# Optimization experiments

Measured on AMD Instinct MI355X. Metric: run time of the kernel, lower is better.

The kernel has to match this reference:

```python
import jax, jax.numpy as jnp
import numpy as np
import math

N_DRUG, N_DIS, D, EMB, HEADS, STEPS = 3072, 3072, 64, 16, 4, 5
N = N_DRUG + N_DIS


def setup_inputs() -> dict:
    key = jax.random.key(0)
    ks = jax.random.split(key, 16)
    s = lambda fan: 1.0 / np.sqrt(fan)
    return {
        "graph": jax.random.uniform(ks[0], (N, N), jnp.float32),
        "drug_f": jax.random.normal(ks[1], (N_DRUG, D), jnp.float32),
        "disease_f": jax.random.normal(ks[2], (N_DIS, D), jnp.float32),
        "timesteps": jax.random.randint(ks[3], (N,), 0, STEPS, jnp.int32),
        "drug_w": jax.random.normal(ks[4], (D, D), jnp.float32) * s(D),
        "disease_w": jax.random.normal(ks[5], (D, D), jnp.float32) * s(D),
        "emb_w": jax.random.normal(ks[6], (EMB, EMB), jnp.float32) * s(EMB),
        "emb_b": jnp.zeros((EMB,), jnp.float32),
        "in_w": jax.random.normal(ks[7], (D + EMB, 256), jnp.float32) * s(D + EMB),
        "in_b": jnp.zeros((256,), jnp.float32),
        "out_w": jax.random.normal(ks[8], (256, D), jnp.float32) * s(256),
        "out_b": jnp.zeros((D,), jnp.float32),
        "wq": jax.random.normal(ks[9], (D, D), jnp.float32) * s(D),
        "bq": jnp.zeros((D,), jnp.float32),
        "wk": jax.random.normal(ks[10], (D, D), jnp.float32) * s(D),
        "bk": jnp.zeros((D,), jnp.float32),
        "wv": jax.random.normal(ks[11], (D, D), jnp.float32) * s(D),
        "bv": jnp.zeros((D,), jnp.float32),
        "wo": jax.random.normal(ks[12], (D, D), jnp.float32) * s(D),
        "bo": jnp.zeros((D,), jnp.float32),
        "fuse_w": jax.random.normal(ks[13], (2 * D, D), jnp.float32) * s(2 * D),
        "fuse_b": jnp.zeros((D,), jnp.float32),
        "ln_g": jnp.ones((D,), jnp.float32),
        "ln_b": jnp.zeros((D,), jnp.float32),
    }


def _layernorm(x, g, b, eps=1e-5):
    mu = jnp.mean(x, axis=-1, keepdims=True)
    var = jnp.var(x, axis=-1, keepdims=True)
    return (x - mu) * jax.lax.rsqrt(var + eps) * g + b


def reference(graph, drug_f, disease_f, timesteps, drug_w, disease_w,
              emb_w, emb_b, in_w, in_b, out_w, out_b,
              wq, bq, wk, bk, wv, bv, wo, bo,
              fuse_w, fuse_b, ln_g, ln_b):
    # ---- DGLLayer: per-type projection + symmetric degree-norm propagation ----
    node_f = jnp.concatenate([drug_f @ drug_w, disease_f @ disease_w], axis=0)  # [N, D]
    degs = jnp.clip(jnp.sum(graph, axis=1), 1.0, None)
    norm = jax.lax.rsqrt(degs)[:, None]  # degs^-0.5, [N, 1]
    target = (graph @ (node_f * norm)) * norm

    # ---- Denoise MLP with sinusoidal time embedding ----
    half = EMB // 2
    freqs = jnp.exp(-math.log(10000.0) * jnp.arange(half, dtype=jnp.float32) / half)
    temp = timesteps.astype(jnp.float32)[:, None] * freqs[None]  # [N, half]
    time_emb = jnp.concatenate([jnp.cos(temp), jnp.sin(temp)], axis=-1)  # [N, EMB]
    emb = time_emb @ emb_w + emb_b
    h = jnp.concatenate([target, emb], axis=-1)  # [N, D+EMB]
    h = jnp.tanh(h @ in_w + in_b)  # in-layer
    aux = h @ out_w + out_b        # final out-layer (no tanh)

    # ---- AttentionFusion: cross-attention(target -> aux) + fuse + residual LN ----
    hd = D // HEADS
    q = (target @ wq + bq).reshape(N, HEADS, hd)
    k = (aux @ wk + bk).reshape(N, HEADS, hd)
    v = (aux @ wv + bv).reshape(N, HEADS, hd)
    scores = jnp.einsum('nhd,mhd->hnm', q, k) / np.sqrt(hd)  # [H, N, N]
    attn = jax.nn.softmax(scores, axis=-1)
    attn_out = jnp.einsum('hnm,mhd->nhd', attn, v).reshape(N, D) @ wo + bo
    fused = jnp.concatenate([target, attn_out], axis=-1) @ fuse_w + fuse_b
    return _layernorm(fused + target, ln_g, ln_b)
```

## Files before the change

### kernel.cpp

```cpp
#include <hip/hip_runtime.h>
#include <cstdint>
#include <cstddef>

#define NTOT 6144
#define NDRUG 3072
#define NM (NTOT*64)

typedef __fp16 f16;
typedef __attribute__((ext_vector_type(2))) __fp16 f16x2;
typedef __attribute__((ext_vector_type(4))) __fp16 f16x4;
typedef __attribute__((ext_vector_type(8))) __fp16 f16x8;
typedef __attribute__((ext_vector_type(4))) float f32x4;

__device__ __forceinline__ f16x8 pack8(float4 a, float4 b){
  f16x2 p0 = __builtin_amdgcn_cvt_pkrtz(a.x, a.y);
  f16x2 p1 = __builtin_amdgcn_cvt_pkrtz(a.z, a.w);
  f16x2 p2 = __builtin_amdgcn_cvt_pkrtz(b.x, b.y);
  f16x2 p3 = __builtin_amdgcn_cvt_pkrtz(b.z, b.w);
  f16x4 lo = __builtin_shufflevector(p0, p1, 0, 1, 2, 3);
  f16x4 hi = __builtin_shufflevector(p2, p3, 0, 1, 2, 3);
  return __builtin_shufflevector(lo, hi, 0, 1, 2, 3, 4, 5, 6, 7);
}

__global__ __launch_bounds__(256) void k_deg(const float* __restrict__ g,
                                             const float* __restrict__ drug_f,
                                             const float* __restrict__ dis_f,
                                             const float* __restrict__ drug_w,
                                             const float* __restrict__ dis_w,
                                             float* __restrict__ norm,
                                             f16* __restrict__ nfst){
  __shared__ float sx[4][64];
  __shared__ float snf[4][64];
  int wv = threadIdx.x >> 6, j = threadIdx.x & 63;
  int row = blockIdx.x*4 + wv;
  const float4* p = (const float4*)(g + (size_t)row * NTOT);
  float s = 0.f;
  #pragma unroll
  for (int it = 0; it < 24; ++it) {
    float4 u = p[it*64 + j];
    s += (u.x + u.y) + (u.z + u.w);
  }
  #pragma unroll
  for (int off = 32; off; off >>= 1) s += __shfl_xor(s, off, 64);
  float nrm = rsqrtf(fmaxf(s, 1.0f));
  if (j == 0) norm[row] = nrm;

  const float* x; const float* W;
  if (row < NDRUG){ x = drug_f + (size_t)row*64; W = drug_w; }
  else            { x = dis_f + (size_t)(row-NDRUG)*64; W = dis_w; }
  sx[wv][j] = x[j];
  __syncthreads();
  float acc = 0.f;
  #pragma unroll 8
  for (int k = 0; k < 64; ++k) acc = fmaf(sx[wv][k], W[k*64+j], acc);
  snf[wv][j] = acc * nrm;
  __syncthreads();
  if (threadIdx.x < 64){
    int c = threadIdx.x;
    f16x4 pk = {(f16)snf[0][c], (f16)snf[1][c], (f16)snf[2][c], (f16)snf[3][c]};
    *(f16x4*)(nfst + (size_t)c*NTOT + blockIdx.x*4) = pk;
  }
}

__global__ __launch_bounds__(256) void k_gemm(const float* __restrict__ graph,
                                              const f16* __restrict__ nfst,
                                              float* __restrict__ part){
  __shared__ f16 sA[2][64][72];
  __shared__ f16 sB[2][64][72];
  const int tid = threadIdx.x;
  const int lane = tid & 63, w = tid >> 6;
  const int l15 = lane & 15, quad = lane >> 4;
  const int row0 = blockIdx.x * 64;
  const int kbase = blockIdx.y * 768;
  const int sr = tid >> 2, scg = (tid & 3) * 16;

  f32x4 acc[4] = {{0.f,0.f,0.f,0.f},{0.f,0.f,0.f,0.f},
                  {0.f,0.f,0.f,0.f},{0.f,0.f,0.f,0.f}};
  float4 a0, a1, a2, a3;
  f16x8 rb0, rb1;
  auto LOADT = [&](int kt){
    const float4* pa = (const float4*)(graph + (size_t)(row0 + sr)*NTOT + kbase + kt*64 + scg);
    a0 = pa[0]; a1 = pa[1]; a2 = pa[2]; a3 = pa[3];
    const f16* pb = nfst + (size_t)sr*NTOT + kbase + kt*64 + scg;
    rb0 = *(const f16x8*)pb; rb1 = *(const f16x8*)(pb + 8);
  };
  auto WRITET = [&](int b){
    *(f16x8*)&sA[b][sr][scg]     = pack8(a0, a1);
    *(f16x8*)&sA[b][sr][scg + 8] = pack8(a2, a3);
    *(f16x8*)&sB[b][sr][scg]     = rb0;
    *(f16x8*)&sB[b][sr][scg + 8] = rb1;
  };
  LOADT(0); WRITET(0);
  int cur = 0;
  for (int kt = 0; kt < 12; ++kt){
    if (kt < 11) LOADT(kt + 1);
    __syncthreads();
    #pragma unroll
    for (int k16 = 0; k16 < 4; ++k16){
      f16x4 af = *(const f16x4*)&sA[cur][w*16 + l15][k16*16 + quad*4];
      #pragma unroll
      for (int nt = 0; nt < 4; ++nt){
        f16x4 bf = *(const f16x4*)&sB[cur][nt*16 + l15][k16*16 + quad*4];
        acc[nt] = __builtin_amdgcn_mfma_f32_16x16x16f16(af, bf, acc[nt], 0, 0, 0);
      }
    }
    if (kt < 11) WRITET(cur ^ 1);
    cur ^= 1;
  }
  float* dst = part + (size_t)blockIdx.y * NM;
  #pragma unroll
  for (int nt = 0; nt < 4; ++nt){
    #pragma unroll
    for (int r = 0; r < 4; ++r){
      int row = row0 + w*16 + quad*4 + r;
      dst[(size_t)row*64 + nt*16 + l15] = acc[nt][r];
    }
  }
}

__global__ __launch_bounds__(256) void k_node2(const float* __restrict__ part,
                                               const float* __restrict__ norm,
                                               const int* __restrict__ ts,
                                               const float* __restrict__ emb_w,
                                               const float* __restrict__ emb_b,
                                               const float* __restrict__ in_w,
                                               const float* __restrict__ in_b,
                                               const float* __restrict__ out_w,
                                               const float* __restrict__ out_b,
                                               const float* __restrict__ wq, const float* __restrict__ bq,
                                               const float* __restrict__ wk, const float* __restrict__ bk,
                                               const float* __restrict__ wvw, const float* __restrict__ bv,
                                               float* __restrict__ target,
                                               f16* __restrict__ qh, f16* __restrict__ kh,
                                               f16* __restrict__ vt){
  __shared__ float sx[4][80];
  __shared__ float sh[4][256];
  __shared__ float sa[4][64];
  __shared__ float sv[4][64];
  int wv = threadIdx.x>>6, j = threadIdx.x&63;
  int row = blockIdx.x*4 + wv;

  float t = 0.f;
  #pragma unroll
  for (int p = 0; p < 8; ++p) t += part[(size_t)p*NM + (size_t)row*64 + j];
  t *= norm[row];
  target[(size_t)row*64 + j] = t;
  sx[wv][j] = t;
  if (j < 16) {
    const float FREQ[8] = {1.0f, 0.316227766016838f, 0.1f, 0.0316227766016838f,
                           0.01f, 0.00316227766016838f, 0.001f, 0.000316227766016838f};
    float tt = (float)ts[row];
    float e = emb_b[j];
    #pragma unroll
    for (int k = 0; k < 8; ++k) {
      float a = tt * FREQ[k];
      e = fmaf(cosf(a), emb_w[k*16 + j], e);
      e = fmaf(sinf(a), emb_w[(8+k)*16 + j], e);
    }
    sx[wv][64 + j] = e;
  }
  __syncthreads();
  float a0 = in_b[4*j+0], a1 = in_b[4*j+1], a2 = in_b[4*j+2], a3 = in_b[4*j+3];
  #pragma unroll 8
  for (int k = 0; k < 80; ++k) {
    float xv = sx[wv][k];
    float4 w = *(const float4*)(in_w + k*256 + 4*j);
    a0 = fmaf(xv, w.x, a0);
    a1 = fmaf(xv, w.y, a1);
    a2 = fmaf(xv, w.z, a2);
    a3 = fmaf(xv, w.w, a3);
  }
  sh[wv][4*j+0] = tanhf(a0); sh[wv][4*j+1] = tanhf(a1);
  sh[wv][4*j+2] = tanhf(a2); sh[wv][4*j+3] = tanhf(a3);
  __syncthreads();
  float o = out_b[j];
  #pragma unroll 8
  for (int k = 0; k < 256; ++k) o = fmaf(sh[wv][k], out_w[k*64 + j], o);
  sa[wv][j] = o;
  __syncthreads();
  float q = bq[j], kk = bk[j], vv = bv[j];
  #pragma unroll 8
  for (int k = 0; k < 64; ++k) {
    float tv = sx[wv][k], av = sa[wv][k];
    q  = fmaf(tv, wq[k*64+j],  q);
    kk = fmaf(av, wk[k*64+j],  kk);
    vv = fmaf(av, wvw[k*64+j], vv);
  }
  qh[(size_t)row*64+j] = (f16)(q * 0.360673760222241f);
  kh[(size_t)row*64+j] = (f16)kk;
  sv[wv][j] = vv;
  __syncthreads();
  if (threadIdx.x < 64){
    int c = threadIdx.x;
    f16x4 pk = {(f16)sv[0][c], (f16)sv[1][c], (f16)sv[2][c], (f16)sv[3][c]};
    *(f16x4*)(vt + (size_t)c*NTOT + blockIdx.x*4) = pk;
  }
}

__global__ __launch_bounds__(256) void k_attn(const f16* __restrict__ qh,
                                              const f16* __restrict__ kh,
                                              const f16* __restrict__ vt,
                                              float* __restrict__ opart,
                                              float* __restrict__ lpart){
  __shared__ f16 sK[2][64][72];
  __shared__ f16 sV[2][64][72];
  const int tid = threadIdx.x;
  const int h = tid >> 6;
  const int lane = tid & 63;
  const int l15 = lane & 15, quad = lane >> 4;
  const int z = blockIdx.y;
  const int q0 = blockIdx.x * 64;

  f16x4 qf[4];
  #pragma unroll
  for (int qn = 0; qn < 4; ++qn)
    qf[qn] = *(const f16x4*)(qh + (size_t)(q0 + qn*16 + l15)*64 + h*16 + quad*4);

  f32x4 accOT[4] = {{0.f,0.f,0.f,0.f},{0.f,0.f,0.f,0.f},
                    {0.f,0.f,0.f,0.f},{0.f,0.f,0.f,0.f}};
  float lsum[4] = {0.f, 0.f, 0.f, 0.f};
  const int sr = tid >> 2, scg = (tid & 3) * 16;
  const int kbase = z * 768;
  f16x8 rk0, rk1, rv0, rv1;
  auto LOADT = [&](int kt){
    const int k0 = kbase + kt*64;
    const f16* pk = kh + (size_t)(k0 + sr)*64 + scg;
    rk0 = *(const f16x8*)pk; rk1 = *(const f16x8*)(pk + 8);
    const f16* pv = vt + (size_t)sr*NTOT + k0 + scg;
    rv0 = *(const f16x8*)pv; rv1 = *(const f16x8*)(pv + 8);
  };
  auto WRITET = [&](int b){
    *(f16x8*)&sK[b][sr][scg]     = rk0;
    *(f16x8*)&sK[b][sr][scg + 8] = rk1;
    *(f16x8*)&sV[b][sr][scg]     = rv0;
    *(f16x8*)&sV[b][sr][scg + 8] = rv1;
  };
  LOADT(0); WRITET(0);
  int cur = 0;
  for (int kt = 0; kt < 12; ++kt){
    if (kt < 11) LOADT(kt + 1);
    __syncthreads();
    #pragma unroll
    for (int km = 0; km < 4; ++km){
      f16x4 kf = *(const f16x4*)&sK[cur][km*16 + l15][h*16 + quad*4];
      f16x4 vf = *(const f16x4*)&sV[cur][h*16 + l15][km*16 + quad*4];
      #pragma unroll
      for (int qn = 0; qn < 4; ++qn){
        f32x4 s = __builtin_amdgcn_mfma_f32_16x16x16f16(
            kf, qf[qn], (f32x4){0.f,0.f,0.f,0.f}, 0, 0, 0);
        float p0 = exp2f(fminf(s[0], 14.4269504088896f));
        float p1 = exp2f(fminf(s[1], 14.4269504088896f));
        float p2 = exp2f(fminf(s[2], 14.4269504088896f));
        float p3 = exp2f(fminf(s[3], 14.4269504088896f));
        lsum[qn] += (p0 + p1) + (p2 + p3);
        f16x2 plo = __builtin_amdgcn_cvt_pkrtz(p0, p1);
        f16x2 phi = __builtin_amdgcn_cvt_pkrtz(p2, p3);
        f16x4 pf = __builtin_shufflevector(plo, phi, 0, 1, 2, 3);
        accOT[qn] = __builtin_amdgcn_mfma_f32_16x16x16f16(vf, pf, accOT[qn], 0, 0, 0);
      }
    }
    if (kt < 11) WRITET(cur ^ 1);
    cur ^= 1;
  }
  #pragma unroll
  for (int qn = 0; qn < 4; ++qn){
    lsum[qn] += __shfl_xor(lsum[qn], 16, 64);
    lsum[qn] += __shfl_xor(lsum[qn], 32, 64);
  }
  #pragma unroll
  for (int qn = 0; qn < 4; ++qn){
    const int row = q0 + qn*16 + l15;
    *(float4*)(opart + (size_t)z*NM + (size_t)row*64 + h*16 + quad*4) =
        make_float4(accOT[qn][0], accOT[qn][1], accOT[qn][2], accOT[qn][3]);
    if (quad == 0) lpart[((size_t)z*4 + h)*NTOT + row] = lsum[qn];
  }
}

__global__ __launch_bounds__(256) void k_out(const float* __restrict__ opart,
                                             const float* __restrict__ lpart,
                                             const float* __restrict__ target,
                                             const float* __restrict__ wo, const float* __restrict__ bo,
                                             const float* __restrict__ fuse_w, const float* __restrict__ fuse_b,
                                             const float* __restrict__ ln_g, const float* __restrict__ ln_b,
                                             float* __restrict__ out){
  __shared__ float st[4][64], sa[4][64], sao[4][64];
  int wv = threadIdx.x>>6, j = threadIdx.x&63;
  int row = blockIdx.x*4 + wv;
  int h = j >> 4;
  float osum = 0.f, L = 0.f;
  #pragma unroll
  for (int z = 0; z < 8; ++z) {
    osum += opart[(size_t)z*NM + (size_t)row*64 + j];
    L    += lpart[((size_t)z*4 + h)*NTOT + row];
  }
  sa[wv][j] = osum / L;
  st[wv][j] = target[(size_t)row*64+j];
  __syncthreads();
  float ao = bo[j];
  #pragma unroll 8
  for (int k = 0; k < 64; ++k) ao = fmaf(sa[wv][k], wo[k*64+j], ao);
  sao[wv][j] = ao;
  __syncthreads();
  float f = fuse_b[j];
  #pragma unroll 8
  for (int k = 0; k < 64; ++k) f = fmaf(st[wv][k], fuse_w[k*64+j], f);
  #pragma unroll 8
  for (int k = 0; k < 64; ++k) f = fmaf(sao[wv][k], fuse_w[(64+k)*64+j], f);
  float x = f + st[wv][j];
  float s1 = x, s2 = x*x;
  #pragma unroll
  for (int off = 32; off; off >>= 1) { s1 += __shfl_xor(s1, off, 64); s2 += __shfl_xor(s2, off, 64); }
  float mu = s1*(1.f/64.f);
  float var = s2*(1.f/64.f) - mu*mu;
  float y = (x-mu)*rsqrtf(var + 1e-5f)*ln_g[j] + ln_b[j];
  out[(size_t)row*64 + j] = y;
}

extern "C" void kernel_launch(void* const* d_in, const int* in_sizes, int n_in,
                              void* d_out, int out_size, void* d_ws, size_t ws_size,
                              hipStream_t stream) {
  const float* graph  = (const float*)d_in[0];
  const float* drug_f = (const float*)d_in[1];
  const float* dis_f  = (const float*)d_in[2];
  const int*   ts     = (const int*)d_in[3];
  const float* drug_w = (const float*)d_in[4];
  const float* dis_w  = (const float*)d_in[5];
  const float* emb_w  = (const float*)d_in[6];
  const float* emb_b  = (const float*)d_in[7];
  const float* in_w   = (const float*)d_in[8];
  const float* in_b   = (const float*)d_in[9];
  const float* out_w  = (const float*)d_in[10];
  const float* out_b  = (const float*)d_in[11];
  const float* wq     = (const float*)d_in[12];
  const float* bq     = (const float*)d_in[13];
  const float* wk     = (const float*)d_in[14];
  const float* bk     = (const float*)d_in[15];
  const float* wvw    = (const float*)d_in[16];
  const float* bv     = (const float*)d_in[17];
  const float* wo     = (const float*)d_in[18];
  const float* bo     = (const float*)d_in[19];
  const float* fuse_w = (const float*)d_in[20];
  const float* fuse_b = (const float*)d_in[21];
  const float* ln_g   = (const float*)d_in[22];
  const float* ln_b   = (const float*)d_in[23];

  float* ws     = (float*)d_ws;
  float* norm   = ws;
  f16*   nfst   = (f16*)(ws + 8192);
  float* target = ws + 8192 + (size_t)64*NTOT/2;
  f16*   qh     = (f16*)(target + NM);
  f16*   kh     = (f16*)(target + NM + NM/2);
  f16*   vt     = (f16*)(target + NM + NM);
  float* part   = target + NM + NM + NM/2;
  float* opart  = part + (size_t)8*NM;
  float* lpart  = opart + (size_t)8*NM;

  k_deg<<<1536, 256, 0, stream>>>(graph, drug_f, dis_f, drug_w, dis_w, norm, nfst);
  k_gemm<<<dim3(96, 8), 256, 0, stream>>>(graph, nfst, part);
  k_node2<<<1536, 256, 0, stream>>>(part, norm, ts, emb_w, emb_b, in_w, in_b,
                                    out_w, out_b, wq, bq, wk, bk, wvw, bv,
                                    target, qh, kh, vt);
  k_attn<<<dim3(96, 8), 256, 0, stream>>>(qh, kh, vt, opart, lpart);
  k_out<<<1536, 256, 0, stream>>>(opart, lpart, target, wo, bo, fuse_w, fuse_b,
                                  ln_g, ln_b, (float*)d_out);
}
```

Before: 400.7 us.

## Fuse degree and propagation GEMM with per-slice atomic readiness barrier

Merges the degree/projection kernel and the graph GEMM into one persistent-style kernel. Each block computes norm and projected features for 8 rows, then signals an atomic counter for its K-slice and spins until all 96 producer blocks of that slice are done before running the GEMM on that slice. Both the GEMM and attention loops are also restructured to hold two register-staged tiles in flight, deepening prefetch. This removes a kernel launch boundary and lets slices start early, but depends on all 768 blocks being co-resident (launch_bounds 256,3) to avoid deadlock, and adds register pressure.

```diff
diff --git a/kernel.cpp b/kernel.cpp
--- a/kernel.cpp
+++ b/kernel.cpp
@@ -22,98 +22,135 @@
   return __builtin_shufflevector(lo, hi, 0, 1, 2, 3, 4, 5, 6, 7);
 }
 
-__global__ __launch_bounds__(256) void k_deg(const float* __restrict__ g,
-                                             const float* __restrict__ drug_f,
-                                             const float* __restrict__ dis_f,
-                                             const float* __restrict__ drug_w,
-                                             const float* __restrict__ dis_w,
-                                             float* __restrict__ norm,
-                                             f16* __restrict__ nfst){
-  __shared__ float sx[4][64];
-  __shared__ float snf[4][64];
-  int wv = threadIdx.x >> 6, j = threadIdx.x & 63;
-  int row = blockIdx.x*4 + wv;
-  const float4* p = (const float4*)(g + (size_t)row * NTOT);
-  float s = 0.f;
-  #pragma unroll
-  for (int it = 0; it < 24; ++it) {
-    float4 u = p[it*64 + j];
-    s += (u.x + u.y) + (u.z + u.w);
-  }
-  #pragma unroll
-  for (int off = 32; off; off >>= 1) s += __shfl_xor(s, off, 64);
-  float nrm = rsqrtf(fmaxf(s, 1.0f));
-  if (j == 0) norm[row] = nrm;
-
-  const float* x; const float* W;
-  if (row < NDRUG){ x = drug_f + (size_t)row*64; W = drug_w; }
-  else            { x = dis_f + (size_t)(row-NDRUG)*64; W = dis_w; }
-  sx[wv][j] = x[j];
-  __syncthreads();
-  float acc = 0.f;
-  #pragma unroll 8
-  for (int k = 0; k < 64; ++k) acc = fmaf(sx[wv][k], W[k*64+j], acc);
-  snf[wv][j] = acc * nrm;
-  __syncthreads();
-  if (threadIdx.x < 64){
-    int c = threadIdx.x;
-    f16x4 pk = {(f16)snf[0][c], (f16)snf[1][c], (f16)snf[2][c], (f16)snf[3][c]};
-    *(f16x4*)(nfst + (size_t)c*NTOT + blockIdx.x*4) = pk;
-  }
-}
-
-__global__ __launch_bounds__(256) void k_gemm(const float* __restrict__ graph,
-                                              const f16* __restrict__ nfst,
-                                              float* __restrict__ part){
-  __shared__ f16 sA[2][64][72];
-  __shared__ f16 sB[2][64][72];
+__global__ __launch_bounds__(256, 3) void k_dg(const float* __restrict__ graph,
+                                               const float* __restrict__ drug_f,
+                                               const float* __restrict__ dis_f,
+                                               const float* __restrict__ drug_w,
+                                               const float* __restrict__ dis_w,
+                                               float* __restrict__ norm,
+                                               f16* __restrict__ nfst,
+                                               float* __restrict__ part,
+                                               unsigned* __restrict__ ready){
+  __shared__ __align__(16) char smem[36864];
   const int tid = threadIdx.x;
-  const int lane = tid & 63, w = tid >> 6;
-  const int l15 = lane & 15, quad = lane >> 4;
-  const int row0 = blockIdx.x * 64;
-  const int kbase = blockIdx.y * 768;
-  const int sr = tid >> 2, scg = (tid & 3) * 16;
-
-  f32x4 acc[4] = {{0.f,0.f,0.f,0.f},{0.f,0.f,0.f,0.f},
-                  {0.f,0.f,0.f,0.f},{0.f,0.f,0.f,0.f}};
-  float4 a0, a1, a2, a3;
-  f16x8 rb0, rb1;
-  auto LOADT = [&](int kt){
-    const float4* pa = (const float4*)(graph + (size_t)(row0 + sr)*NTOT + kbase + kt*64 + scg);
-    a0 = pa[0]; a1 = pa[1]; a2 = pa[2]; a3 = pa[3];
-    const f16* pb = nfst + (size_t)sr*NTOT + kbase + kt*64 + scg;
-    rb0 = *(const f16x8*)pb; rb1 = *(const f16x8*)(pb + 8);
-  };
-  auto WRITET = [&](int b){
-    *(f16x8*)&sA[b][sr][scg]     = pack8(a0, a1);
-    *(f16x8*)&sA[b][sr][scg + 8] = pack8(a2, a3);
-    *(f16x8*)&sB[b][sr][scg]     = rb0;
-    *(f16x8*)&sB[b][sr][scg + 8] = rb1;
-  };
-  LOADT(0); WRITET(0);
-  int cur = 0;
-  for (int kt = 0; kt < 12; ++kt){
-    if (kt < 11) LOADT(kt + 1);
-    __syncthreads();
+  const int bx = blockIdx.x;
+  const int wv = tid >> 6, j = tid & 63;
+
+  {
+    float (*sx)[64]  = (float(*)[64])smem;
+    float (*snf)[64] = (float(*)[64])(smem + 1024);
+    for (int half = 0; half < 2; ++half){
+      const int bi = bx*2 + half;
+      const int row = bi*4 + wv;
+      const float4* p = (const float4*)(graph + (size_t)row * NTOT);
+      float s = 0.f;
+      #pragma unroll
+      for (int it = 0; it < 24; ++it) {
+        float4 u = p[it*64 + j];
+        s += (u.x + u.y) + (u.z + u.w);
+      }
+      #pragma unroll
+      for (int off = 32; off; off >>= 1) s += __shfl_xor(s, off, 64);
+      float nrm = rsqrtf(fmaxf(s, 1.0f));
+      if (j == 0) norm[row] = nrm;
+
+      const float* x; const float* W;
+      if (row < NDRUG){ x = drug_f + (size_t)row*64; W = drug_w; }
+      else            { x = dis_f + (size_t)(row-NDRUG)*64; W = dis_w; }
+      sx[wv][j] = x[j];
+      __syncthreads();
+      float acc = 0.f;
+      #pragma unroll 8
+      for (int k = 0; k < 64; ++k) acc = fmaf(sx[wv][k], W[k*64+j], acc);
+      snf[wv][j] = acc * nrm;
+      __syncthreads();
+      if (tid < 64){
+        int c = tid;
+        f16x4 pk = {(f16)snf[0][c], (f16)snf[1][c], (f16)snf[2][c], (f16)snf[3][c]};
+        *(f16x4*)(nfst + (size_t)c*NTOT + bi*4) = pk;
+      }
+      __syncthreads();
+    }
+  }
+
+  const int z = bx / 96;
+  if (tid == 0){
+    __threadfence();
+    __hip_atomic_fetch_add(ready + z, 1u, __ATOMIC_ACQ_REL, __HIP_MEMORY_SCOPE_AGENT);
+    while (__hip_atomic_load(ready + z, __ATOMIC_ACQUIRE, __HIP_MEMORY_SCOPE_AGENT) < 96u)
+      __builtin_amdgcn_s_sleep(2);
+    __threadfence();
+  }
+  __syncthreads();
+
+  {
+    typedef f16 (*TileP)[64][72];
+    TileP sA = (TileP)smem;
+    TileP sB = (TileP)(smem + 18432);
+    const int lane = tid & 63, w = tid >> 6;
+    const int l15 = lane & 15, quad = lane >> 4;
+    const int row0 = (bx % 96) * 64;
+    const int kbase = z * 768;
+    const int sr = tid >> 2, scg = (tid & 3) * 16;
+
+    f32x4 acc[4] = {{0.f,0.f,0.f,0.f},{0.f,0.f,0.f,0.f},
+                    {0.f,0.f,0.f,0.f},{0.f,0.f,0.f,0.f}};
+    float4 aA0, aA1, aA2, aA3, aB0, aB1, aB2, aB3;
+    f16x8 bA0, bA1, bB0, bB1;
+    auto LOADA = [&](int kt){
+      const float4* pa = (const float4*)(graph + (size_t)(row0 + sr)*NTOT + kbase + kt*64 + scg);
+      aA0 = pa[0]; aA1 = pa[1]; aA2 = pa[2]; aA3 = pa[3];
+      const f16* pb = nfst + (size_t)sr*NTOT + kbase + kt*64 + scg;
+      bA0 = *(const f16x8*)pb; bA1 = *(const f16x8*)(pb + 8);
+    };
+    auto LOADB = [&](int kt){
+      const float4* pa = (const float4*)(graph + (size_t)(row0 + sr)*NTOT + kbase + kt*64 + scg);
+      aB0 = pa[0]; aB1 = pa[1]; aB2 = pa[2]; aB3 = pa[3];
+      const f16* pb = nfst + (size_t)sr*NTOT + kbase + kt*64 + scg;
+      bB0 = *(const f16x8*)pb; bB1 = *(const f16x8*)(pb + 8);
+    };
+    auto WRA = [&](int b){
+      *(f16x8*)&sA[b][sr][scg]     = pack8(aA0, aA1);
+      *(f16x8*)&sA[b][sr][scg + 8] = pack8(aA2, aA3);
+      *(f16x8*)&sB[b][sr][scg]     = bA0;
+      *(f16x8*)&sB[b][sr][scg + 8] = bA1;
+    };
+    auto WRB = [&](int b){
+      *(f16x8*)&sA[b][sr][scg]     = pack8(aB0, aB1);
+      *(f16x8*)&sA[b][sr][scg + 8] = pack8(aB2, aB3);
+      *(f16x8*)&sB[b][sr][scg]     = bB0;
+      *(f16x8*)&sB[b][sr][scg + 8] = bB1;
+    };
+    auto COMPUTE = [&](int b){
+      #pragma unroll
+      for (int k16 = 0; k16 < 4; ++k16){
+        f16x4 af = *(const f16x4*)&sA[b][w*16 + l15][k16*16 + quad*4];
+        #pragma unroll
+        for (int nt = 0; nt < 4; ++nt){
+          f16x4 bf = *(const f16x4*)&sB[b][nt*16 + l15][k16*16 + quad*4];
+          acc[nt] = __builtin_amdgcn_mfma_f32_16x16x16f16(af, bf, acc[nt], 0, 0, 0);
+        }
+      }
+    };
+    LOADA(0); LOADB(1); WRA(0);
+    for (int kt2 = 0; kt2 < 12; kt2 += 2){
+      if (kt2 + 2 < 12) LOADA(kt2 + 2);
+      __syncthreads();
+      COMPUTE(0);
+      WRB(1);
+      if (kt2 + 3 < 12) LOADB(kt2 + 3);
+      __syncthreads();
+      COMPUTE(1);
+      if (kt2 + 2 < 12) WRA(0);
+    }
+    float* dst = part + (size_t)z * NM;
     #pragma unroll
-    for (int k16 = 0; k16 < 4; ++k16){
-      f16x4 af = *(const f16x4*)&sA[cur][w*16 + l15][k16*16 + quad*4];
+    for (int nt = 0; nt < 4; ++nt){
       #pragma unroll
-      for (int nt = 0; nt < 4; ++nt){
-        f16x4 bf = *(const f16x4*)&sB[cur][nt*16 + l15][k16*16 + quad*4];
-        acc[nt] = __builtin_amdgcn_mfma_f32_16x16x16f16(af, bf, acc[nt], 0, 0, 0);
+      for (int r = 0; r < 4; ++r){
+        int row = row0 + w*16 + quad*4 + r;
+        dst[(size_t)row*64 + nt*16 + l15] = acc[nt][r];
       }
-    }
-    if (kt < 11) WRITET(cur ^ 1);
-    cur ^= 1;
-  }
-  float* dst = part + (size_t)blockIdx.y * NM;
-  #pragma unroll
-  for (int nt = 0; nt < 4; ++nt){
-    #pragma unroll
-    for (int r = 0; r < 4; ++r){
-      int row = row0 + w*16 + quad*4 + r;
-      dst[(size_t)row*64 + nt*16 + l15] = acc[nt][r];
     }
   }
 }
@@ -221,29 +258,38 @@
   float lsum[4] = {0.f, 0.f, 0.f, 0.f};
   const int sr = tid >> 2, scg = (tid & 3) * 16;
   const int kbase = z * 768;
-  f16x8 rk0, rk1, rv0, rv1;
-  auto LOADT = [&](int kt){
+  f16x8 kA0, kA1, vA0, vA1, kB0, kB1, vB0, vB1;
+  auto LOADA = [&](int kt){
     const int k0 = kbase + kt*64;
     const f16* pk = kh + (size_t)(k0 + sr)*64 + scg;
-    rk0 = *(const f16x8*)pk; rk1 = *(const f16x8*)(pk + 8);
+    kA0 = *(const f16x8*)pk; kA1 = *(const f16x8*)(pk + 8);
     const f16* pv = vt + (size_t)sr*NTOT + k0 + scg;
-    rv0 = *(const f16x8*)pv; rv1 = *(const f16x8*)(pv + 8);
+    vA0 = *(const f16x8*)pv; vA1 = *(const f16x8*)(pv + 8);
   };
-  auto WRITET = [&](int b){
-    *(f16x8*)&sK[b][sr][scg]     = rk0;
-    *(f16x8*)&sK[b][sr][scg + 8] = rk1;
-    *(f16x8*)&sV[b][sr][scg]     = rv0;
-    *(f16x8*)&sV[b][sr][scg + 8] = rv1;
+  auto LOADB = [&](int kt){
+    const int k0 = kbase + kt*64;
+    const f16* pk = kh + (size_t)(k0 + sr)*64 + scg;
+    kB0 = *(const f16x8*)pk; kB1 = *(const f16x8*)(pk + 8);
+    const f16* pv = vt + (size_t)sr*NTOT + k0 + scg;
+    vB0 = *(const f16x8*)pv; vB1 = *(const f16x8*)(pv + 8);
   };
-  LOADT(0); WRITET(0);
-  int cur = 0;
-  for (int kt = 0; kt < 12; ++kt){
-    if (kt < 11) LOADT(kt + 1);
-    __syncthreads();
+  auto WRA = [&](int b){
+    *(f16x8*)&sK[b][sr][scg]     = kA0;
+    *(f16x8*)&sK[b][sr][scg + 8] = kA1;
+    *(f16x8*)&sV[b][sr][scg]     = vA0;
+    *(f16x8*)&sV[b][sr][scg + 8] = vA1;
+  };
+  auto WRB = [&](int b){
+    *(f16x8*)&sK[b][sr][scg]     = kB0;
+    *(f16x8*)&sK[b][sr][scg + 8] = kB1;
+    *(f16x8*)&sV[b][sr][scg]     = vB0;
+    *(f16x8*)&sV[b][sr][scg + 8] = vB1;
+  };
+  auto COMPUTE = [&](int b){
     #pragma unroll
     for (int km = 0; km < 4; ++km){
-      f16x4 kf = *(const f16x4*)&sK[cur][km*16 + l15][h*16 + quad*4];
-      f16x4 vf = *(const f16x4*)&sV[cur][h*16 + l15][km*16 + quad*4];
+      f16x4 kf = *(const f16x4*)&sK[b][km*16 + l15][h*16 + quad*4];
+      f16x4 vf = *(const f16x4*)&sV[b][h*16 + l15][km*16 + quad*4];
       #pragma unroll
       for (int qn = 0; qn < 4; ++qn){
         f32x4 s = __builtin_amdgcn_mfma_f32_16x16x16f16(
@@ -259,8 +305,17 @@
         accOT[qn] = __builtin_amdgcn_mfma_f32_16x16x16f16(vf, pf, accOT[qn], 0, 0, 0);
       }
     }
-    if (kt < 11) WRITET(cur ^ 1);
-    cur ^= 1;
+  };
+  LOADA(0); LOADB(1); WRA(0);
+  for (int kt2 = 0; kt2 < 12; kt2 += 2){
+    if (kt2 + 2 < 12) LOADA(kt2 + 2);
+    __syncthreads();
+    COMPUTE(0);
+    WRB(1);
+    if (kt2 + 3 < 12) LOADB(kt2 + 3);
+    __syncthreads();
+    COMPUTE(1);
+    if (kt2 + 2 < 12) WRA(0);
   }
   #pragma unroll
   for (int qn = 0; qn < 4; ++qn){
@@ -344,19 +399,21 @@
   const float* ln_g   = (const float*)d_in[22];
   const float* ln_b   = (const float*)d_in[23];
 
-  float* ws     = (float*)d_ws;
-  float* norm   = ws;
-  f16*   nfst   = (f16*)(ws + 8192);
-  float* target = ws + 8192 + (size_t)64*NTOT/2;
-  f16*   qh     = (f16*)(target + NM);
-  f16*   kh     = (f16*)(target + NM + NM/2);
-  f16*   vt     = (f16*)(target + NM + NM);
-  float* part   = target + NM + NM + NM/2;
-  float* opart  = part + (size_t)8*NM;
-  float* lpart  = opart + (size_t)8*NM;
-
-  k_deg<<<1536, 256, 0, stream>>>(graph, drug_f, dis_f, drug_w, dis_w, norm, nfst);
-  k_gemm<<<dim3(96, 8), 256, 0, stream>>>(graph, nfst, part);
+  float*    ws     = (float*)d_ws;
+  float*    norm   = ws;
+  unsigned* ready  = (unsigned*)(ws + 6656);
+  f16*      nfst   = (f16*)(ws + 8192);
+  float*    target = ws + 8192 + (size_t)64*NTOT/2;
+  f16*      qh     = (f16*)(target + NM);
+  f16*      kh     = (f16*)(target + NM + NM/2);
+  f16*      vt     = (f16*)(target + NM + NM);
+  float*    part   = target + NM + NM + NM/2;
+  float*    opart  = part + (size_t)8*NM;
+  float*    lpart  = opart + (size_t)8*NM;
+
+  hipMemsetAsync((void*)ready, 0, 32, stream);
+  k_dg<<<768, 256, 0, stream>>>(graph, drug_f, dis_f, drug_w, dis_w,
+                                norm, nfst, part, ready);
   k_node2<<<1536, 256, 0, stream>>>(part, norm, ts, emb_w, emb_b, in_w, in_b,
                                     out_w, out_b, wq, bq, wk, bk, wvw, bv,
                                     target, qh, kh, vt);
```

After: 512.1 us. +27.8%, slower.
